# Optimization experiments

Measured on AMD Instinct MI355X. Metric: run time of the kernel, lower is better.

Reference implementation:

```python
import jax, jax.numpy as jnp
import numpy as np

N = 50000      # nodes
E = 800000     # edges
F_IN = 64      # num_node_features
H = 128        # hidden_channels
C = 2          # num_classes
G = 16         # graphs in batch


def setup_inputs() -> dict:
    key = jax.random.key(0)
    ks = jax.random.split(key, 16)
    def lin(k, fan_in, shape):
        return jax.random.normal(k, shape, jnp.float32) / np.sqrt(fan_in)
    return {
        "x": jax.random.normal(ks[0], (N, F_IN), jnp.float32),
        "edge_index": jax.random.randint(ks[1], (2, E), 0, N, dtype=jnp.int32),
        "batch": jnp.sort(jax.random.randint(ks[2], (N,), 0, G, dtype=jnp.int32)),
        "W1": lin(ks[3], F_IN, (F_IN, H)), "b1": jnp.zeros((H,), jnp.float32),
        "W2": lin(ks[4], H, (H, H)),       "b2": jnp.zeros((H,), jnp.float32),
        "W3": lin(ks[5], H, (H, H)),       "b3": jnp.zeros((H,), jnp.float32),
        "W4": lin(ks[6], H, (H, H)),       "b4": jnp.zeros((H,), jnp.float32),
        "lw1": lin(ks[7], H, (H, H // 2)), "lb1": jnp.zeros((H // 2,), jnp.float32),
        "lw2": lin(ks[8], H // 2, (H // 2, C)), "lb2": jnp.zeros((C,), jnp.float32),
    }


def _graph_norm(edge_index):
    # PyG GCNConv default: add self-loops, symmetric normalization.
    loop = jnp.arange(N, dtype=edge_index.dtype)
    src = jnp.concatenate([edge_index[0], loop])  # message source
    dst = jnp.concatenate([edge_index[1], loop])  # aggregation target
    deg = jax.ops.segment_sum(jnp.ones_like(dst, jnp.float32), dst, num_segments=N)
    dinv = jnp.where(deg > 0, jax.lax.rsqrt(deg), 0.0)
    norm = dinv[src] * dinv[dst]                  # [E+N]
    return src, dst, norm


def _gcn_conv(h, W, b, src, dst, norm):
    hw = h @ W                                    # [N, out]
    msg = hw[src] * norm[:, None]                 # gather + normalize  [E+N, out]
    agg = jax.ops.segment_sum(msg, dst, num_segments=N)  # scatter-add
    return agg + b


def reference(x, edge_index, batch, W1, b1, W2, b2, W3, b3, W4, b4, lw1, lb1, lw2, lb2):
    src, dst, norm = _graph_norm(edge_index)
    h = jax.nn.relu(_gcn_conv(x, W1, b1, src, dst, norm))   # dropout inactive (eval)
    h = jax.nn.relu(_gcn_conv(h, W2, b2, src, dst, norm))
    h = jax.nn.relu(_gcn_conv(h, W3, b3, src, dst, norm))
    h = _gcn_conv(h, W4, b4, src, dst, norm)
    # global_mean_pool over graph ids
    cnt = jax.ops.segment_sum(jnp.ones((N,), jnp.float32), batch, num_segments=G)
    pooled = jax.ops.segment_sum(h, batch, num_segments=G) / jnp.maximum(cnt, 1.0)[:, None]
    out = jax.nn.relu(pooled @ lw1 + lb1)
    return out @ lw2 + lb2
```

## Files before the change

### kernel.cpp

```cpp
#include <hip/hip_runtime.h>

#define NN 50000
#define NPAD 50048
#define NE 800000
#define FIN 64
#define H 128
#define NG 16
#define NPART 64
#define NBUCK 196
#define BUCK_CAP 4800
#define FILLA_BLOCKS 512
#define FILLA_CHUNK 1563
#define ROW_U 64
#define DUMMY NN
#define ZERO_I4 32768
#define PREP_ITEMS (NPAD * FIN + H * FIN + 3 * H * H + ZERO_I4)
#define PREP_BLOCKS ((PREP_ITEMS + 255) / 256)

typedef __bf16 bf16x8 __attribute__((ext_vector_type(8)));
typedef float f32x4 __attribute__((ext_vector_type(4)));
typedef float f32x2 __attribute__((ext_vector_type(2)));
typedef unsigned int u32x4 __attribute__((ext_vector_type(4)));

__device__ inline unsigned short bf16r(float x) {
    unsigned int u = __float_as_uint(x);
    return (unsigned short)((u + 0x7fffu + ((u >> 16) & 1u)) >> 16);
}
__device__ inline unsigned int pack_bf16x2(float a, float b) {
    return (unsigned int)bf16r(a) | ((unsigned int)bf16r(b) << 16);
}
__device__ inline float bf_lo(unsigned int u) { return __uint_as_float(u << 16); }
__device__ inline float bf_hi(unsigned int u) { return __uint_as_float(u & 0xffff0000u); }

__device__ inline void pkadd(f32x2& a, unsigned int u) {
    f32x2 p;
    p.x = bf_lo(u);
    p.y = bf_hi(u);
    asm("v_pk_add_f32 %0, %1, %0" : "+v"(a) : "v"(p));
}
__device__ inline void bfly(f32x2& a, int m) {
    a.x += __shfl_xor(a.x, m);
    a.y += __shfl_xor(a.y, m);
}

__global__ __launch_bounds__(256) void fillA_prep_kernel(const int* __restrict__ ei,
                                                         int* __restrict__ gcount,
                                                         unsigned int* __restrict__ ebuf,
                                                         const float* __restrict__ x,
                                                         const float* __restrict__ W1,
                                                         const float* __restrict__ W2,
                                                         const float* __restrict__ W3,
                                                         const float* __restrict__ W4,
                                                         unsigned short* __restrict__ xb,
                                                         unsigned short* __restrict__ Wt1,
                                                         unsigned short* __restrict__ Wt2,
                                                         unsigned short* __restrict__ Wt3,
                                                         unsigned short* __restrict__ Wt4,
                                                         int4* __restrict__ zbuf) {
    const int t = threadIdx.x;
    if (blockIdx.x >= FILLA_BLOCKS) {
        int e = (blockIdx.x - FILLA_BLOCKS) * 256 + t;
        if (e < NPAD * FIN) {
            int n = e >> 6;
            xb[e] = (n < NN) ? bf16r(x[e]) : (unsigned short)0;
            return;
        }
        int tt = e - NPAD * FIN;
        if (tt < H * FIN) {
            int n = tt / FIN, k = tt % FIN;
            Wt1[tt] = bf16r(W1[k * H + n]);
            return;
        }
        int u = tt - H * FIN;
        if (u < 3 * H * H) {
            const float* W = W2;
            unsigned short* Wt = Wt2;
            if (u >= 2 * H * H) { W = W4; Wt = Wt4; u -= 2 * H * H; }
            else if (u >= H * H) { W = W3; Wt = Wt3; u -= H * H; }
            int n = u / H, k = u % H;
            Wt[u] = bf16r(W[k * H + n]);
            return;
        }
        int z = u - 3 * H * H;
        if (z < ZERO_I4) zbuf[z] = make_int4(0, 0, 0, 0);
        return;
    }
    __shared__ int hist[256];
    __shared__ int base[256];
    hist[t] = 0;
    __syncthreads();
    const int e0 = blockIdx.x * FILLA_CHUNK;
    const int e1 = min(e0 + FILLA_CHUNK, NE);
    for (int e = e0 + t; e < e1; e += 256)
        atomicAdd(&hist[ei[NE + e] >> 8], 1);
    __syncthreads();
    {
        int h = hist[t];
        base[t] = h ? atomicAdd(&gcount[t], h) : 0;
    }
    __syncthreads();
    for (int e = e0 + t; e < e1; e += 256) {
        int d = ei[NE + e];
        int s = ei[e];
        int b = d >> 8;
        int pos = atomicAdd(&base[b], 1);
        ebuf[b * BUCK_CAP + pos] = (unsigned int)s | ((unsigned int)d << 16);
    }
}

__global__ __launch_bounds__(256) void fillB_kernel(const unsigned int* __restrict__ ebuf,
                                                    const int* __restrict__ gcount,
                                                    int* __restrict__ galloc,
                                                    int* __restrict__ pcnt,
                                                    const int* __restrict__ batch,
                                                    int2* __restrict__ rowse,
                                                    float* __restrict__ dinv,
                                                    unsigned short* __restrict__ csr) {
    __shared__ int lh[256];
    __shared__ int lsum[256];
    __shared__ int lcur[256];
    __shared__ int lgc[16];
    __shared__ int base_s;
    const int b = blockIdx.x, t = threadIdx.x;
    const int n0 = b * 256;
    lh[t] = 0;
    if (t < 16) lgc[t] = 0;
    __syncthreads();
    const int ne = gcount[b];
    const unsigned int* __restrict__ eb = ebuf + b * BUCK_CAP;
    for (int i = t; i < ne; i += 256)
        atomicAdd(&lh[(int)(eb[i] >> 16) - n0], 1);
    __syncthreads();
    const int c = lh[t];
    const int p = (c + 7) & ~7;
    const int n = n0 + t;
    if (n < NN) atomicAdd(&lgc[batch[n]], 1);
    lsum[t] = p;
    __syncthreads();
    if (t < 16 && lgc[t]) atomicAdd(&pcnt[t], lgc[t]);
    for (int off = 1; off < 256; off <<= 1) {
        int u = (t >= off) ? lsum[t - off] : 0;
        __syncthreads();
        lsum[t] += u;
        __syncthreads();
    }
    if (t == 255) base_s = atomicAdd(galloc, lsum[255]);
    const int excl = t ? lsum[t - 1] : 0;
    __syncthreads();
    const int st = base_s + excl;
    if (n < NN) {
        rowse[n] = make_int2(st, st + p);
        dinv[n] = rsqrtf((float)c + 1.0f);
    } else if (n < NPAD) {
        rowse[n] = make_int2(0, 0);
        dinv[n] = 0.0f;
    }
    lcur[t] = st;
    __syncthreads();
    for (int i = t; i < ne; i += 256) {
        unsigned int u = eb[i];
        int pos = atomicAdd(&lcur[(int)(u >> 16) - n0], 1);
        csr[pos] = (unsigned short)(u & 0xFFFFu);
    }
    __syncthreads();
    for (int k = st + c; k < st + p; k++) csr[k] = (unsigned short)DUMMY;
}

#define LSTRIDE 130
template <int K>
__global__ __launch_bounds__(256) void gemm_mfma_kernel(const unsigned short* __restrict__ hb,
                                                        const unsigned short* __restrict__ Wt,
                                                        const float* __restrict__ dinv,
                                                        unsigned int* __restrict__ outu) {
    __shared__ float ls[64 * LSTRIDE];
    const int wave = threadIdx.x >> 6, lane = threadIdx.x & 63;
    const int m15 = lane & 15, quad = lane >> 4;
    const int row0 = blockIdx.x * 64;
    const int arow = row0 + wave * 16 + m15;

    bf16x8 a[K / 32];
#pragma unroll
    for (int ks = 0; ks < K / 32; ks++)
        a[ks] = *(const bf16x8*)&hb[(size_t)arow * K + ks * 32 + quad * 8];

    const int lrow = wave * 16 + quad * 4;
    float dv[4];
#pragma unroll
    for (int r = 0; r < 4; r++) dv[r] = dinv[row0 + lrow + r];

#pragma unroll
    for (int ct = 0; ct < 8; ct++) {
        f32x4 acc = {0.f, 0.f, 0.f, 0.f};
#pragma unroll
        for (int ks = 0; ks < K / 32; ks++) {
            bf16x8 b = *(const bf16x8*)&Wt[(ct * 16 + m15) * K + ks * 32 + quad * 8];
            acc = __builtin_amdgcn_mfma_f32_16x16x32_bf16(a[ks], b, acc, 0, 0, 0);
        }
#pragma unroll
        for (int r = 0; r < 4; r++)
            ls[(lrow + r) * LSTRIDE + ct * 16 + m15] = acc[r] * dv[r];
    }
    __syncthreads();

#pragma unroll
    for (int k = 0; k < 4; k++) {
        int idx = threadIdx.x + 256 * k;
        int row = idx >> 4, q = idx & 15;
        const float* p = &ls[row * LSTRIDE + q * 8];
        u32x4 o;
        o[0] = pack_bf16x2(p[0], p[1]);
        o[1] = pack_bf16x2(p[2], p[3]);
        o[2] = pack_bf16x2(p[4], p[5]);
        o[3] = pack_bf16x2(p[6], p[7]);
        __builtin_nontemporal_store(
            o, (u32x4*)&outu[(size_t)(row0 + row) * ROW_U + q * 4]);
    }
}

__device__ inline void gather_row(const unsigned int* __restrict__ hwc,
                                  const int2* __restrict__ rowse,
                                  const unsigned short* __restrict__ csr,
                                  int n, int u0,
                                  f32x2& a0, f32x2& a1, f32x2& a2, f32x2& a3) {
    uint4 sv = *(const uint4*)&hwc[(size_t)n * ROW_U + u0];
    a0.x = bf_lo(sv.x); a0.y = bf_hi(sv.x);
    a1.x = bf_lo(sv.y); a1.y = bf_hi(sv.y);
    a2.x = bf_lo(sv.z); a2.y = bf_hi(sv.z);
    a3.x = bf_lo(sv.w); a3.y = bf_hi(sv.w);
    const int2 se = rowse[n];
    int i = se.x;
    for (; i + 16 <= se.y; i += 16) {
        u32x4 c0 = __builtin_nontemporal_load((const u32x4*)&csr[i]);
        u32x4 c1 = __builtin_nontemporal_load((const u32x4*)&csr[i + 8]);
        int s0 = c0[0] & 0xFFFF, s1 = c0[0] >> 16;
        int s2 = c0[1] & 0xFFFF, s3 = c0[1] >> 16;
        int s4 = c0[2] & 0xFFFF, s5 = c0[2] >> 16;
        int s6 = c0[3] & 0xFFFF, s7 = c0[3] >> 16;
        int t0 = c1[0] & 0xFFFF, t1 = c1[0] >> 16;
        int t2 = c1[1] & 0xFFFF, t3 = c1[1] >> 16;
        int t4 = c1[2] & 0xFFFF, t5 = c1[2] >> 16;
        int t6 = c1[3] & 0xFFFF, t7 = c1[3] >> 16;
        uint4 v0 = *(const uint4*)&hwc[(size_t)s0 * ROW_U + u0];
        uint4 v1 = *(const uint4*)&hwc[(size_t)s1 * ROW_U + u0];
        uint4 v2 = *(const uint4*)&hwc[(size_t)s2 * ROW_U + u0];
        uint4 v3 = *(const uint4*)&hwc[(size_t)s3 * ROW_U + u0];
        uint4 v4 = *(const uint4*)&hwc[(size_t)s4 * ROW_U + u0];
        uint4 v5 = *(const uint4*)&hwc[(size_t)s5 * ROW_U + u0];
        uint4 v6 = *(const uint4*)&hwc[(size_t)s6 * ROW_U + u0];
        uint4 v7 = *(const uint4*)&hwc[(size_t)s7 * ROW_U + u0];
        uint4 w0 = *(const uint4*)&hwc[(size_t)t0 * ROW_U + u0];
        uint4 w1 = *(const uint4*)&hwc[(size_t)t1 * ROW_U + u0];
        uint4 w2 = *(const uint4*)&hwc[(size_t)t2 * ROW_U + u0];
        uint4 w3 = *(const uint4*)&hwc[(size_t)t3 * ROW_U + u0];
        uint4 w4 = *(const uint4*)&hwc[(size_t)t4 * ROW_U + u0];
        uint4 w5 = *(const uint4*)&hwc[(size_t)t5 * ROW_U + u0];
        uint4 w6 = *(const uint4*)&hwc[(size_t)t6 * ROW_U + u0];
        uint4 w7 = *(const uint4*)&hwc[(size_t)t7 * ROW_U + u0];
        pkadd(a0, v0.x); pkadd(a1, v0.y); pkadd(a2, v0.z); pkadd(a3, v0.w);
        pkadd(a0, v1.x); pkadd(a1, v1.y); pkadd(a2, v1.z); pkadd(a3, v1.w);
        pkadd(a0, v2.x); pkadd(a1, v2.y); pkadd(a2, v2.z); pkadd(a3, v2.w);
        pkadd(a0, v3.x); pkadd(a1, v3.y); pkadd(a2, v3.z); pkadd(a3, v3.w);
        pkadd(a0, v4.x); pkadd(a1, v4.y); pkadd(a2, v4.z); pkadd(a3, v4.w);
        pkadd(a0, v5.x); pkadd(a1, v5.y); pkadd(a2, v5.z); pkadd(a3, v5.w);
        pkadd(a0, v6.x); pkadd(a1, v6.y); pkadd(a2, v6.z); pkadd(a3, v6.w);
        pkadd(a0, v7.x); pkadd(a1, v7.y); pkadd(a2, v7.z); pkadd(a3, v7.w);
        pkadd(a0, w0.x); pkadd(a1, w0.y); pkadd(a2, w0.z); pkadd(a3, w0.w);
        pkadd(a0, w1.x); pkadd(a1, w1.y); pkadd(a2, w1.z); pkadd(a3, w1.w);
        pkadd(a0, w2.x); pkadd(a1, w2.y); pkadd(a2, w2.z); pkadd(a3, w2.w);
        pkadd(a0, w3.x); pkadd(a1, w3.y); pkadd(a2, w3.z); pkadd(a3, w3.w);
        pkadd(a0, w4.x); pkadd(a1, w4.y); pkadd(a2, w4.z); pkadd(a3, w4.w);
        pkadd(a0, w5.x); pkadd(a1, w5.y); pkadd(a2, w5.z); pkadd(a3, w5.w);
        pkadd(a0, w6.x); pkadd(a1, w6.y); pkadd(a2, w6.z); pkadd(a3, w6.w);
        pkadd(a0, w7.x); pkadd(a1, w7.y); pkadd(a2, w7.z); pkadd(a3, w7.w);
    }
    if (i < se.y) {
        u32x4 c = __builtin_nontemporal_load((const u32x4*)&csr[i]);
        int s0 = c[0] & 0xFFFF, s1 = c[0] >> 16;
        int s2 = c[1] & 0xFFFF, s3 = c[1] >> 16;
        int s4 = c[2] & 0xFFFF, s5 = c[2] >> 16;
        int s6 = c[3] & 0xFFFF, s7 = c[3] >> 16;
        uint4 v0 = *(const uint4*)&hwc[(size_t)s0 * ROW_U + u0];
        uint4 v1 = *(const uint4*)&hwc[(size_t)s1 * ROW_U + u0];
        uint4 v2 = *(const uint4*)&hwc[(size_t)s2 * ROW_U + u0];
        uint4 v3 = *(const uint4*)&hwc[(size_t)s3 * ROW_U + u0];
        uint4 v4 = *(const uint4*)&hwc[(size_t)s4 * ROW_U + u0];
        uint4 v5 = *(const uint4*)&hwc[(size_t)s5 * ROW_U + u0];
        uint4 v6 = *(const uint4*)&hwc[(size_t)s6 * ROW_U + u0];
        uint4 v7 = *(const uint4*)&hwc[(size_t)s7 * ROW_U + u0];
        pkadd(a0, v0.x); pkadd(a1, v0.y); pkadd(a2, v0.z); pkadd(a3, v0.w);
        pkadd(a0, v1.x); pkadd(a1, v1.y); pkadd(a2, v1.z); pkadd(a3, v1.w);
        pkadd(a0, v2.x); pkadd(a1, v2.y); pkadd(a2, v2.z); pkadd(a3, v2.w);
        pkadd(a0, v3.x); pkadd(a1, v3.y); pkadd(a2, v3.z); pkadd(a3, v3.w);
        pkadd(a0, v4.x); pkadd(a1, v4.y); pkadd(a2, v4.z); pkadd(a3, v4.w);
        pkadd(a0, v5.x); pkadd(a1, v5.y); pkadd(a2, v5.z); pkadd(a3, v5.w);
        pkadd(a0, v6.x); pkadd(a1, v6.y); pkadd(a2, v6.z); pkadd(a3, v6.w);
        pkadd(a0, v7.x); pkadd(a1, v7.y); pkadd(a2, v7.z); pkadd(a3, v7.w);
    }
}

template <int MODE>
__global__ __launch_bounds__(256) void agg_kernel(const unsigned int* __restrict__ hwc,
                                                  const int2* __restrict__ rowse,
                                                  const unsigned short* __restrict__ csr,
                                                  const float* __restrict__ dinv,
                                                  const float* __restrict__ bias,
                                                  const int* __restrict__ batch,
                                                  float* __restrict__ poolpart,
                                                  unsigned int* __restrict__ outc) {
    const int u = threadIdx.x & 15;
    const int u0 = u * 4;
    if (MODE == 0) {
        const int n = blockIdx.x * 16 + (threadIdx.x >> 4);
        f32x2 a0, a1, a2, a3;
        gather_row(hwc, rowse, csr, n, u0, a0, a1, a2, a3);
        const float d = dinv[n];
        const float2* bp = (const float2*)bias + u0;
        float2 q0 = bp[0], q1 = bp[1], q2 = bp[2], q3 = bp[3];
        u32x4 o;
        o[0] = pack_bf16x2(fmaxf(a0.x * d + q0.x, 0.f), fmaxf(a0.y * d + q0.y, 0.f));
        o[1] = pack_bf16x2(fmaxf(a1.x * d + q1.x, 0.f), fmaxf(a1.y * d + q1.y, 0.f));
        o[2] = pack_bf16x2(fmaxf(a2.x * d + q2.x, 0.f), fmaxf(a2.y * d + q2.y, 0.f));
        o[3] = pack_bf16x2(fmaxf(a3.x * d + q3.x, 0.f), fmaxf(a3.y * d + q3.y, 0.f));
        __builtin_nontemporal_store(o, (u32x4*)&outc[(size_t)n * ROW_U + u0]);
        return;
    }
    __shared__ float lds[4][128];
    const int nip = threadIdx.x >> 4;
    const int lane = threadIdx.x & 63, wave = threadIdx.x >> 6;
    const int n0 = blockIdx.x * 64;
    const int copy = blockIdx.x & (NPART - 1);
    const int gfirst0 = batch[n0];
    const bool blockUni = (gfirst0 == batch[min(n0 + 63, NN - 1)]);
    float* __restrict__ ppb = poolpart + copy * (NG * H);
    f32x2 acc0 = {0.f, 0.f}, acc1 = {0.f, 0.f}, acc2 = {0.f, 0.f}, acc3 = {0.f, 0.f};
#pragma unroll
    for (int p = 0; p < 4; p++) {
        const int n = n0 + p * 16 + nip;
        f32x2 t0, t1, t2, t3;
        gather_row(hwc, rowse, csr, n, u0, t0, t1, t2, t3);
        const float d = dinv[n];
        t0 *= d; t1 *= d; t2 *= d; t3 *= d;
        if (blockUni) {
            acc0 += t0; acc1 += t1; acc2 += t2; acc3 += t3;
        } else {
            const int gb = batch[min(n, NN - 1)];
            const bool uni = (__shfl(gb, 0) == __shfl(gb, 63));
            if (uni) {
                bfly(t0, 16); bfly(t1, 16); bfly(t2, 16); bfly(t3, 16);
                bfly(t0, 32); bfly(t1, 32); bfly(t2, 32); bfly(t3, 32);
                if (lane < 16) {
                    float* q = ppb + __shfl(gb, 0) * H + lane * 8;
                    atomicAdd(&q[0], t0.x); atomicAdd(&q[1], t0.y);
                    atomicAdd(&q[2], t1.x); atomicAdd(&q[3], t1.y);
                    atomicAdd(&q[4], t2.x); atomicAdd(&q[5], t2.y);
                    atomicAdd(&q[6], t3.x); atomicAdd(&q[7], t3.y);
                }
            } else if (n < NN) {
                float* q = ppb + gb * H + u * 8;
                atomicAdd(&q[0], t0.x); atomicAdd(&q[1], t0.y);
                atomicAdd(&q[2], t1.x); atomicAdd(&q[3], t1.y);
                atomicAdd(&q[4], t2.x); atomicAdd(&q[5], t2.y);
                atomicAdd(&q[6], t3.x); atomicAdd(&q[7], t3.y);
            }
        }
    }
    if (blockUni) {
        bfly(acc0, 16); bfly(acc1, 16); bfly(acc2, 16); bfly(acc3, 16);
        bfly(acc0, 32); bfly(acc1, 32); bfly(acc2, 32); bfly(acc3, 32);
        if (lane < 16) {
            float* q = &lds[wave][lane * 8];
            q[0] = acc0.x; q[1] = acc0.y;
            q[2] = acc1.x; q[3] = acc1.y;
            q[4] = acc2.x; q[5] = acc2.y;
            q[6] = acc3.x; q[7] = acc3.y;
        }
        __syncthreads();
        if (threadIdx.x < 128) {
            float tot = lds[0][threadIdx.x] + lds[1][threadIdx.x] +
                        lds[2][threadIdx.x] + lds[3][threadIdx.x];
            atomicAdd(&ppb[gfirst0 * H + threadIdx.x], tot);
        }
    }
}

__global__ __launch_bounds__(1024) void mlp_kernel(const float* __restrict__ poolpart,
                                                   const int* __restrict__ pcnt,
                                                   const float* __restrict__ b4,
                                                   const float* __restrict__ lw1,
                                                   const float* __restrict__ lb1,
                                                   const float* __restrict__ lw2,
                                                   const float* __restrict__ lb2,
                                                   float* __restrict__ out) {
    __shared__ float mean_s[NG * H];
    __shared__ float cnt_s[NG];
    __shared__ float hid_s[NG * 64];
    int tid = threadIdx.x;
    if (tid < NG) cnt_s[tid] = fmaxf((float)pcnt[tid], 1.0f);
    __syncthreads();
    for (int i = tid; i < NG * H; i += 1024) {
        float s = 0.f;
        for (int p = 0; p < NPART; p++) s += poolpart[p * (NG * H) + i];
        mean_s[i] = s / cnt_s[i >> 7] + b4[i & (H - 1)];
    }
    __syncthreads();
    {
        int g = tid >> 6, j = tid & 63;
        float acc = lb1[j];
        for (int f = 0; f < H; f++) acc += mean_s[g * H + f] * lw1[f * 64 + j];
        hid_s[g * 64 + j] = fmaxf(acc, 0.f);
    }
    __syncthreads();
    if (tid < 32) {
        int g = tid >> 1, c = tid & 1;
        float acc = lb2[c];
        for (int j = 0; j < 64; j++) acc += hid_s[g * 64 + j] * lw2[j * 2 + c];
        out[g * 2 + c] = acc;
    }
}

extern "C" void kernel_launch(void* const* d_in, const int* in_sizes, int n_in,
                              void* d_out, int out_size, void* d_ws, size_t ws_size,
                              hipStream_t stream) {
    const float* x = (const float*)d_in[0];
    const int* ei = (const int*)d_in[1];
    const int* batch = (const int*)d_in[2];
    const float* W1 = (const float*)d_in[3];
    const float* b1 = (const float*)d_in[4];
    const float* W2 = (const float*)d_in[5];
    const float* b2 = (const float*)d_in[6];
    const float* W3 = (const float*)d_in[7];
    const float* b3 = (const float*)d_in[8];
    const float* W4 = (const float*)d_in[9];
    const float* b4 = (const float*)d_in[10];
    const float* lw1 = (const float*)d_in[11];
    const float* lb1 = (const float*)d_in[12];
    const float* lw2 = (const float*)d_in[13];
    const float* lb2 = (const float*)d_in[14];
    float* out = (float*)d_out;

    int* wsi = (int*)d_ws;
    int* gcount = wsi;
    int* galloc = wsi + 256;
    int* pcnt = wsi + 280;
    float* poolpart = (float*)(wsi + 512);
    int2* rowse = (int2*)(wsi + 131584);
    unsigned short* csr = (unsigned short*)(wsi + 231680);
    float* dinv = (float*)(wsi + 831680);
    unsigned short* Wt1 = (unsigned short*)(wsi + 881728);
    unsigned short* Wt2 = (unsigned short*)(wsi + 885824);
    unsigned short* Wt3 = (unsigned short*)(wsi + 894016);
    unsigned short* Wt4 = (unsigned short*)(wsi + 902208);
    unsigned short* xb = (unsigned short*)(wsi + 910400);
    unsigned int* hb = (unsigned int*)(wsi + 2511936);
    unsigned int* hwb = (unsigned int*)(wsi + 5715008);
    unsigned int* ebuf = (unsigned int*)(wsi + 8918080);

    const int gemmBlocks = NPAD / 64;
    const int agg0Blocks = NPAD / 16;
    const int agg1Blocks = NPAD / 64;

    hipMemsetAsync(wsi, 0, 512 * sizeof(int), stream);
    fillA_prep_kernel<<<FILLA_BLOCKS + PREP_BLOCKS, 256, 0, stream>>>(
        ei, gcount, ebuf, x, W1, W2, W3, W4, xb, Wt1, Wt2, Wt3, Wt4, (int4*)poolpart);
    fillB_kernel<<<NBUCK, 256, 0, stream>>>(ebuf, gcount, galloc, pcnt, batch,
                                            rowse, dinv, csr);

    gemm_mfma_kernel<FIN><<<gemmBlocks, 256, 0, stream>>>(xb, Wt1, dinv, hwb);
    agg_kernel<0><<<agg0Blocks, 256, 0, stream>>>(hwb, rowse, csr, dinv, b1, batch,
                                                  nullptr, hb);
    gemm_mfma_kernel<H><<<gemmBlocks, 256, 0, stream>>>((unsigned short*)hb, Wt2, dinv, hwb);
    agg_kernel<0><<<agg0Blocks, 256, 0, stream>>>(hwb, rowse, csr, dinv, b2, batch,
                                                  nullptr, hb);
    gemm_mfma_kernel<H><<<gemmBlocks, 256, 0, stream>>>((unsigned short*)hb, Wt3, dinv, hwb);
    agg_kernel<0><<<agg0Blocks, 256, 0, stream>>>(hwb, rowse, csr, dinv, b3, batch,
                                                  nullptr, hb);
    gemm_mfma_kernel<H><<<gemmBlocks, 256, 0, stream>>>((unsigned short*)hb, Wt4, dinv, hwb);
    agg_kernel<1><<<agg1Blocks, 256, 0, stream>>>(hwb, rowse, csr, dinv, nullptr, batch,
                                                  poolpart, nullptr);

    mlp_kernel<<<1, 1024, 0, stream>>>(poolpart, pcnt, b4, lw1, lb1, lw2, lb2, out);
}
```

Measured before the change: 313.8 us.

## Reorder GCN layers: aggregate before transform on first layer, move W4 after pooling

```diff
diff --git a/kernel.cpp b/kernel.cpp
--- a/kernel.cpp
+++ b/kernel.cpp
@@ -12,9 +12,10 @@
 #define FILLA_BLOCKS 512
 #define FILLA_CHUNK 1563
 #define ROW_U 64
+#define XROW_U 32
 #define DUMMY NN
 #define ZERO_I4 32768
-#define PREP_ITEMS (NPAD * FIN + H * FIN + 3 * H * H + ZERO_I4)
+#define PREP_ITEMS (H * FIN + 2 * H * H + ZERO_I4)
 #define PREP_BLOCKS ((PREP_ITEMS + 255) / 256)
 
 typedef __bf16 bf16x8 __attribute__((ext_vector_type(8)));
@@ -46,42 +47,31 @@
 __global__ __launch_bounds__(256) void fillA_prep_kernel(const int* __restrict__ ei,
                                                          int* __restrict__ gcount,
                                                          unsigned int* __restrict__ ebuf,
-                                                         const float* __restrict__ x,
                                                          const float* __restrict__ W1,
                                                          const float* __restrict__ W2,
                                                          const float* __restrict__ W3,
-                                                         const float* __restrict__ W4,
-                                                         unsigned short* __restrict__ xb,
                                                          unsigned short* __restrict__ Wt1,
                                                          unsigned short* __restrict__ Wt2,
                                                          unsigned short* __restrict__ Wt3,
-                                                         unsigned short* __restrict__ Wt4,
                                                          int4* __restrict__ zbuf) {
     const int t = threadIdx.x;
     if (blockIdx.x >= FILLA_BLOCKS) {
         int e = (blockIdx.x - FILLA_BLOCKS) * 256 + t;
-        if (e < NPAD * FIN) {
-            int n = e >> 6;
-            xb[e] = (n < NN) ? bf16r(x[e]) : (unsigned short)0;
+        if (e < H * FIN) {
+            int n = e / FIN, k = e % FIN;
+            Wt1[e] = bf16r(W1[k * H + n]);
             return;
         }
-        int tt = e - NPAD * FIN;
-        if (tt < H * FIN) {
-            int n = tt / FIN, k = tt % FIN;
-            Wt1[tt] = bf16r(W1[k * H + n]);
-            return;
-        }
-        int u = tt - H * FIN;
-        if (u < 3 * H * H) {
+        int u = e - H * FIN;
+        if (u < 2 * H * H) {
             const float* W = W2;
             unsigned short* Wt = Wt2;
-            if (u >= 2 * H * H) { W = W4; Wt = Wt4; u -= 2 * H * H; }
-            else if (u >= H * H) { W = W3; Wt = Wt3; u -= H * H; }
+            if (u >= H * H) { W = W3; Wt = Wt3; u -= H * H; }
             int n = u / H, k = u % H;
             Wt[u] = bf16r(W[k * H + n]);
             return;
         }
-        int z = u - 3 * H * H;
+        int z = u - 2 * H * H;
         if (z < ZERO_I4) zbuf[z] = make_int4(0, 0, 0, 0);
         return;
     }
@@ -166,11 +156,30 @@
     for (int k = st + c; k < st + p; k++) csr[k] = (unsigned short)DUMMY;
 }
 
+__global__ __launch_bounds__(256) void xprep_kernel(const float* __restrict__ x,
+                                                    const float* __restrict__ dinv,
+                                                    unsigned short* __restrict__ xb) {
+    const int idx = blockIdx.x * 256 + threadIdx.x;
+    const int e4 = idx * 4;
+    const int n = e4 >> 6;
+    uint2 o;
+    if (n < NN) {
+        float4 v = *(const float4*)&x[e4];
+        float d = dinv[n];
+        o.x = pack_bf16x2(v.x * d, v.y * d);
+        o.y = pack_bf16x2(v.z * d, v.w * d);
+    } else {
+        o.x = o.y = 0u;
+    }
+    *(uint2*)&xb[e4] = o;
+}
+
 #define LSTRIDE 130
-template <int K>
+template <int K, int EPI>
 __global__ __launch_bounds__(256) void gemm_mfma_kernel(const unsigned short* __restrict__ hb,
                                                         const unsigned short* __restrict__ Wt,
                                                         const float* __restrict__ dinv,
+                                                        const float* __restrict__ bias,
                                                         unsigned int* __restrict__ outu) {
     __shared__ float ls[64 * LSTRIDE];
     const int wave = threadIdx.x >> 6, lane = threadIdx.x & 63;
@@ -185,8 +194,10 @@
 
     const int lrow = wave * 16 + quad * 4;
     float dv[4];
-#pragma unroll
-    for (int r = 0; r < 4; r++) dv[r] = dinv[row0 + lrow + r];
+    if (EPI == 0) {
+#pragma unroll
+        for (int r = 0; r < 4; r++) dv[r] = dinv[row0 + lrow + r];
+    }
 
 #pragma unroll
     for (int ct = 0; ct < 8; ct++) {
@@ -196,9 +207,12 @@
             bf16x8 b = *(const bf16x8*)&Wt[(ct * 16 + m15) * K + ks * 32 + quad * 8];
             acc = __builtin_amdgcn_mfma_f32_16x16x32_bf16(a[ks], b, acc, 0, 0, 0);
         }
-#pragma unroll
-        for (int r = 0; r < 4; r++)
-            ls[(lrow + r) * LSTRIDE + ct * 16 + m15] = acc[r] * dv[r];
+        float bv = (EPI == 1) ? bias[ct * 16 + m15] : 0.f;
+#pragma unroll
+        for (int r = 0; r < 4; r++) {
+            float v = (EPI == 0) ? acc[r] * dv[r] : fmaxf(acc[r] + bv, 0.f);
+            ls[(lrow + r) * LSTRIDE + ct * 16 + m15] = v;
+        }
     }
     __syncthreads();
 
@@ -212,17 +226,19 @@
         o[1] = pack_bf16x2(p[2], p[3]);
         o[2] = pack_bf16x2(p[4], p[5]);
         o[3] = pack_bf16x2(p[6], p[7]);
+        if (EPI == 1 && row0 + row >= NN) { o[0] = o[1] = o[2] = o[3] = 0u; }
         __builtin_nontemporal_store(
             o, (u32x4*)&outu[(size_t)(row0 + row) * ROW_U + q * 4]);
     }
 }
 
+template <int RU>
 __device__ inline void gather_row(const unsigned int* __restrict__ hwc,
                                   const int2* __restrict__ rowse,
                                   const unsigned short* __restrict__ csr,
                                   int n, int u0,
                                   f32x2& a0, f32x2& a1, f32x2& a2, f32x2& a3) {
-    uint4 sv = *(const uint4*)&hwc[(size_t)n * ROW_U + u0];
+    uint4 sv = *(const uint4*)&hwc[(size_t)n * RU + u0];
     a0.x = bf_lo(sv.x); a0.y = bf_hi(sv.x);
     a1.x = bf_lo(sv.y); a1.y = bf_hi(sv.y);
     a2.x = bf_lo(sv.z); a2.y = bf_hi(sv.z);
@@ -240,22 +256,22 @@
         int t2 = c1[1] & 0xFFFF, t3 = c1[1] >> 16;
         int t4 = c1[2] & 0xFFFF, t5 = c1[2] >> 16;
         int t6 = c1[3] & 0xFFFF, t7 = c1[3] >> 16;
-        uint4 v0 = *(const uint4*)&hwc[(size_t)s0 * ROW_U + u0];
-        uint4 v1 = *(const uint4*)&hwc[(size_t)s1 * ROW_U + u0];
-        uint4 v2 = *(const uint4*)&hwc[(size_t)s2 * ROW_U + u0];
-        uint4 v3 = *(const uint4*)&hwc[(size_t)s3 * ROW_U + u0];
-        uint4 v4 = *(const uint4*)&hwc[(size_t)s4 * ROW_U + u0];
-        uint4 v5 = *(const uint4*)&hwc[(size_t)s5 * ROW_U + u0];
-        uint4 v6 = *(const uint4*)&hwc[(size_t)s6 * ROW_U + u0];
-        uint4 v7 = *(const uint4*)&hwc[(size_t)s7 * ROW_U + u0];
-        uint4 w0 = *(const uint4*)&hwc[(size_t)t0 * ROW_U + u0];
-        uint4 w1 = *(const uint4*)&hwc[(size_t)t1 * ROW_U + u0];
-        uint4 w2 = *(const uint4*)&hwc[(size_t)t2 * ROW_U + u0];
-        uint4 w3 = *(const uint4*)&hwc[(size_t)t3 * ROW_U + u0];
-        uint4 w4 = *(const uint4*)&hwc[(size_t)t4 * ROW_U + u0];
-        uint4 w5 = *(const uint4*)&hwc[(size_t)t5 * ROW_U + u0];
-        uint4 w6 = *(const uint4*)&hwc[(size_t)t6 * ROW_U + u0];
-        uint4 w7 = *(const uint4*)&hwc[(size_t)t7 * ROW_U + u0];
+        uint4 v0 = *(const uint4*)&hwc[(size_t)s0 * RU + u0];
+        uint4 v1 = *(const uint4*)&hwc[(size_t)s1 * RU + u0];
+        uint4 v2 = *(const uint4*)&hwc[(size_t)s2 * RU + u0];
+        uint4 v3 = *(const uint4*)&hwc[(size_t)s3 * RU + u0];
+        uint4 v4 = *(const uint4*)&hwc[(size_t)s4 * RU + u0];
+        uint4 v5 = *(const uint4*)&hwc[(size_t)s5 * RU + u0];
+        uint4 v6 = *(const uint4*)&hwc[(size_t)s6 * RU + u0];
+        uint4 v7 = *(const uint4*)&hwc[(size_t)s7 * RU + u0];
+        uint4 w0 = *(const uint4*)&hwc[(size_t)t0 * RU + u0];
+        uint4 w1 = *(const uint4*)&hwc[(size_t)t1 * RU + u0];
+        uint4 w2 = *(const uint4*)&hwc[(size_t)t2 * RU + u0];
+        uint4 w3 = *(const uint4*)&hwc[(size_t)t3 * RU + u0];
+        uint4 w4 = *(const uint4*)&hwc[(size_t)t4 * RU + u0];
+        uint4 w5 = *(const uint4*)&hwc[(size_t)t5 * RU + u0];
+        uint4 w6 = *(const uint4*)&hwc[(size_t)t6 * RU + u0];
+        uint4 w7 = *(const uint4*)&hwc[(size_t)t7 * RU + u0];
         pkadd(a0, v0.x); pkadd(a1, v0.y); pkadd(a2, v0.z); pkadd(a3, v0.w);
         pkadd(a0, v1.x); pkadd(a1, v1.y); pkadd(a2, v1.z); pkadd(a3, v1.w);
         pkadd(a0, v2.x); pkadd(a1, v2.y); pkadd(a2, v2.z); pkadd(a3, v2.w);
@@ -279,14 +295,14 @@
         int s2 = c[1] & 0xFFFF, s3 = c[1] >> 16;
         int s4 = c[2] & 0xFFFF, s5 = c[2] >> 16;
         int s6 = c[3] & 0xFFFF, s7 = c[3] >> 16;
-        uint4 v0 = *(const uint4*)&hwc[(size_t)s0 * ROW_U + u0];
-        uint4 v1 = *(const uint4*)&hwc[(size_t)s1 * ROW_U + u0];
-        uint4 v2 = *(const uint4*)&hwc[(size_t)s2 * ROW_U + u0];
-        uint4 v3 = *(const uint4*)&hwc[(size_t)s3 * ROW_U + u0];
-        uint4 v4 = *(const uint4*)&hwc[(size_t)s4 * ROW_U + u0];
-        uint4 v5 = *(const uint4*)&hwc[(size_t)s5 * ROW_U + u0];
-        uint4 v6 = *(const uint4*)&hwc[(size_t)s6 * ROW_U + u0];
-        uint4 v7 = *(const uint4*)&hwc[(size_t)s7 * ROW_U + u0];
+        uint4 v0 = *(const uint4*)&hwc[(size_t)s0 * RU + u0];
+        uint4 v1 = *(const uint4*)&hwc[(size_t)s1 * RU + u0];
+        uint4 v2 = *(const uint4*)&hwc[(size_t)s2 * RU + u0];
+        uint4 v3 = *(const uint4*)&hwc[(size_t)s3 * RU + u0];
+        uint4 v4 = *(const uint4*)&hwc[(size_t)s4 * RU + u0];
+        uint4 v5 = *(const uint4*)&hwc[(size_t)s5 * RU + u0];
+        uint4 v6 = *(const uint4*)&hwc[(size_t)s6 * RU + u0];
+        uint4 v7 = *(const uint4*)&hwc[(size_t)s7 * RU + u0];
         pkadd(a0, v0.x); pkadd(a1, v0.y); pkadd(a2, v0.z); pkadd(a3, v0.w);
         pkadd(a0, v1.x); pkadd(a1, v1.y); pkadd(a2, v1.z); pkadd(a3, v1.w);
         pkadd(a0, v2.x); pkadd(a1, v2.y); pkadd(a2, v2.z); pkadd(a3, v2.w);
@@ -296,6 +312,24 @@
         pkadd(a0, v6.x); pkadd(a1, v6.y); pkadd(a2, v6.z); pkadd(a3, v6.w);
         pkadd(a0, v7.x); pkadd(a1, v7.y); pkadd(a2, v7.z); pkadd(a3, v7.w);
     }
+}
+
+__global__ __launch_bounds__(256) void aggx_kernel(const unsigned int* __restrict__ xbu,
+                                                   const int2* __restrict__ rowse,
+                                                   const unsigned short* __restrict__ csr,
+                                                   const float* __restrict__ dinv,
+                                                   unsigned int* __restrict__ xa) {
+    const int u0 = (threadIdx.x & 7) * 4;
+    const int n = blockIdx.x * 32 + (threadIdx.x >> 3);
+    f32x2 a0, a1, a2, a3;
+    gather_row<XROW_U>(xbu, rowse, csr, n, u0, a0, a1, a2, a3);
+    const float d = dinv[n];
+    u32x4 o;
+    o[0] = pack_bf16x2(a0.x * d, a0.y * d);
+    o[1] = pack_bf16x2(a1.x * d, a1.y * d);
+    o[2] = pack_bf16x2(a2.x * d, a2.y * d);
+    o[3] = pack_bf16x2(a3.x * d, a3.y * d);
+    __builtin_nontemporal_store(o, (u32x4*)&xa[(size_t)n * XROW_U + u0]);
 }
 
 template <int MODE>
@@ -309,18 +343,26 @@
                                                   unsigned int* __restrict__ outc) {
     const int u = threadIdx.x & 15;
     const int u0 = u * 4;
-    if (MODE == 0) {
+    if (MODE != 1) {
         const int n = blockIdx.x * 16 + (threadIdx.x >> 4);
         f32x2 a0, a1, a2, a3;
-        gather_row(hwc, rowse, csr, n, u0, a0, a1, a2, a3);
+        gather_row<ROW_U>(hwc, rowse, csr, n, u0, a0, a1, a2, a3);
         const float d = dinv[n];
         const float2* bp = (const float2*)bias + u0;
         float2 q0 = bp[0], q1 = bp[1], q2 = bp[2], q3 = bp[3];
+        float r0 = fmaxf(a0.x * d + q0.x, 0.f), r1 = fmaxf(a0.y * d + q0.y, 0.f);
+        float r2 = fmaxf(a1.x * d + q1.x, 0.f), r3 = fmaxf(a1.y * d + q1.y, 0.f);
+        float r4 = fmaxf(a2.x * d + q2.x, 0.f), r5 = fmaxf(a2.y * d + q2.y, 0.f);
+        float r6 = fmaxf(a3.x * d + q3.x, 0.f), r7 = fmaxf(a3.y * d + q3.y, 0.f);
+        if (MODE == 2) {
+            r0 *= d; r1 *= d; r2 *= d; r3 *= d;
+            r4 *= d; r5 *= d; r6 *= d; r7 *= d;
+        }
         u32x4 o;
-        o[0] = pack_bf16x2(fmaxf(a0.x * d + q0.x, 0.f), fmaxf(a0.y * d + q0.y, 0.f));
-        o[1] = pack_bf16x2(fmaxf(a1.x * d + q1.x, 0.f), fmaxf(a1.y * d + q1.y, 0.f));
-        o[2] = pack_bf16x2(fmaxf(a2.x * d + q2.x, 0.f), fmaxf(a2.y * d + q2.y, 0.f));
-        o[3] = pack_bf16x2(fmaxf(a3.x * d + q3.x, 0.f), fmaxf(a3.y * d + q3.y, 0.f));
+        o[0] = pack_bf16x2(r0, r1);
+        o[1] = pack_bf16x2(r2, r3);
+        o[2] = pack_bf16x2(r4, r5);
+        o[3] = pack_bf16x2(r6, r7);
         __builtin_nontemporal_store(o, (u32x4*)&outc[(size_t)n * ROW_U + u0]);
         return;
     }
@@ -337,7 +379,7 @@
     for (int p = 0; p < 4; p++) {
         const int n = n0 + p * 16 + nip;
         f32x2 t0, t1, t2, t3;
-        gather_row(hwc, rowse, csr, n, u0, t0, t1, t2, t3);
+        gather_row<ROW_U>(hwc, rowse, csr, n, u0, t0, t1, t2, t3);
         const float d = dinv[n];
         t0 *= d; t1 *= d; t2 *= d; t3 *= d;
         if (blockUni) {
@@ -385,6 +427,7 @@
 
 __global__ __launch_bounds__(1024) void mlp_kernel(const float* __restrict__ poolpart,
                                                    const int* __restrict__ pcnt,
+                                                   const float* __restrict__ W4,
                                                    const float* __restrict__ b4,
                                                    const float* __restrict__ lw1,
                                                    const float* __restrict__ lb1,
@@ -392,6 +435,7 @@
                                                    const float* __restrict__ lb2,
                                                    float* __restrict__ out) {
     __shared__ float mean_s[NG * H];
+    __shared__ float z_s[NG * H];
     __shared__ float cnt_s[NG];
     __shared__ float hid_s[NG * 64];
     int tid = threadIdx.x;
@@ -400,13 +444,22 @@
     for (int i = tid; i < NG * H; i += 1024) {
         float s = 0.f;
         for (int p = 0; p < NPART; p++) s += poolpart[p * (NG * H) + i];
-        mean_s[i] = s / cnt_s[i >> 7] + b4[i & (H - 1)];
+        mean_s[i] = s / cnt_s[i >> 7];
+    }
+    __syncthreads();
+#pragma unroll
+    for (int r = 0; r < 2; r++) {
+        int i = tid + r * 1024;
+        int g = i >> 7, j = i & (H - 1);
+        float acc = b4[j];
+        for (int f = 0; f < H; f++) acc += mean_s[g * H + f] * W4[f * H + j];
+        z_s[i] = acc;
     }
     __syncthreads();
     {
         int g = tid >> 6, j = tid & 63;
         float acc = lb1[j];
-        for (int f = 0; f < H; f++) acc += mean_s[g * H + f] * lw1[f * 64 + j];
+        for (int f = 0; f < H; f++) acc += z_s[g * H + f] * lw1[f * 64 + j];
         hid_s[g * 64 + j] = fmaxf(acc, 0.f);
     }
     __syncthreads();
@@ -449,34 +502,38 @@
     unsigned short* Wt1 = (unsigned short*)(wsi + 881728);
     unsigned short* Wt2 = (unsigned short*)(wsi + 885824);
     unsigned short* Wt3 = (unsigned short*)(wsi + 894016);
-    unsigned short* Wt4 = (unsigned short*)(wsi + 902208);
     unsigned short* xb = (unsigned short*)(wsi + 910400);
     unsigned int* hb = (unsigned int*)(wsi + 2511936);
     unsigned int* hwb = (unsigned int*)(wsi + 5715008);
     unsigned int* ebuf = (unsigned int*)(wsi + 8918080);
 
     const int gemmBlocks = NPAD / 64;
+    const int xprepBlocks = NPAD * FIN / 1024;
+    const int aggxBlocks = NPAD / 32;
     const int agg0Blocks = NPAD / 16;
-    const int agg1Blocks = NPAD / 64;
+    const int poolBlocks = NPAD / 64;
 
     hipMemsetAsync(wsi, 0, 512 * sizeof(int), stream);
     fillA_prep_kernel<<<FILLA_BLOCKS + PREP_BLOCKS, 256, 0, stream>>>(
-        ei, gcount, ebuf, x, W1, W2, W3, W4, xb, Wt1, Wt2, Wt3, Wt4, (int4*)poolpart);
+        ei, gcount, ebuf, W1, W2, W3, Wt1, Wt2, Wt3, (int4*)poolpart);
     fillB_kernel<<<NBUCK, 256, 0, stream>>>(ebuf, gcount, galloc, pcnt, batch,
                                             rowse, dinv, csr);
 
-    gemm_mfma_kernel<FIN><<<gemmBlocks, 256, 0, stream>>>(xb, Wt1, dinv, hwb);
-    agg_kernel<0><<<agg0Blocks, 256, 0, stream>>>(hwb, rowse, csr, dinv, b1, batch,
-                                                  nullptr, hb);
-    gemm_mfma_kernel<H><<<gemmBlocks, 256, 0, stream>>>((unsigned short*)hb, Wt2, dinv, hwb);
+    xprep_kernel<<<xprepBlocks, 256, 0, stream>>>(x, dinv, xb);
+    aggx_kernel<<<aggxBlocks, 256, 0, stream>>>((const unsigned int*)xb, rowse, csr,
+                                                dinv, hwb);
+    gemm_mfma_kernel<FIN, 1><<<gemmBlocks, 256, 0, stream>>>((unsigned short*)hwb, Wt1,
+                                                             nullptr, b1, hb);
+    gemm_mfma_kernel<H, 0><<<gemmBlocks, 256, 0, stream>>>((unsigned short*)hb, Wt2,
+                                                           dinv, nullptr, hwb);
     agg_kernel<0><<<agg0Blocks, 256, 0, stream>>>(hwb, rowse, csr, dinv, b2, batch,
                                                   nullptr, hb);
-    gemm_mfma_kernel<H><<<gemmBlocks, 256, 0, stream>>>((unsigned short*)hb, Wt3, dinv, hwb);
-    agg_kernel<0><<<agg0Blocks, 256, 0, stream>>>(hwb, rowse, csr, dinv, b3, batch,
+    gemm_mfma_kernel<H, 0><<<gemmBlocks, 256, 0, stream>>>((unsigned short*)hb, Wt3,
+                                                           dinv, nullptr, hwb);
+    agg_kernel<2><<<agg0Blocks, 256, 0, stream>>>(hwb, rowse, csr, dinv, b3, batch,
                                                   nullptr, hb);
-    gemm_mfma_kernel<H><<<gemmBlocks, 256, 0, stream>>>((unsigned short*)hb, Wt4, dinv, hwb);
-    agg_kernel<1><<<agg1Blocks, 256, 0, stream>>>(hwb, rowse, csr, dinv, nullptr, batch,
+    agg_kernel<1><<<poolBlocks, 256, 0, stream>>>(hb, rowse, csr, dinv, nullptr, batch,
                                                   poolpart, nullptr);
 
-    mlp_kernel<<<1, 1024, 0, stream>>>(poolpart, pcnt, b4, lw1, lb1, lw2, lb2, out);
-}
+    mlp_kernel<<<1, 1024, 0, stream>>>(poolpart, pcnt, W4, b4, lw1, lb1, lw2, lb2, out);
+}
```

After: 291.1 us. 1.08x faster.
